# Optimization experiments

Measured on AMD Instinct MI355X. Metric: run time of the kernel, lower is better.

## Reference

```python
import jax, jax.numpy as jnp
import numpy as np

B, T, D = 32, 512, 256
F = 256  # duration_predictor_filter_size
K = 3    # kernel size, padding=1
MEL_MAX = 2304
EPS = 1e-5


def _conv1d(x, w, b):
    # x: [B, T, C_in], w: [C_out, C_in, K], 'same'-ish padding=1
    y = jax.lax.conv_general_dilated(
        x.transpose(0, 2, 1), w, window_strides=(1,), padding=[(1, 1)],
        dimension_numbers=("NCH", "OIH", "NCH"))
    return y.transpose(0, 2, 1) + b


def _layernorm(x, g, b):
    mu = jnp.mean(x, axis=-1, keepdims=True)
    var = jnp.mean(jnp.square(x - mu), axis=-1, keepdims=True)
    return (x - mu) * jax.lax.rsqrt(var + EPS) * g + b


def setup_inputs() -> dict:
    key = jax.random.key(0)
    ks = jax.random.split(key, 8)
    x = jax.random.normal(ks[0], (B, T, D), dtype=jnp.float32)
    target = jax.random.randint(ks[1], (B, T), 0, 8, dtype=jnp.int32)
    s = 0.02
    return {
        "x": x,
        "target": target,
        "mel_max_length": MEL_MAX,
        "conv1_w": jax.random.normal(ks[2], (F, D, K), dtype=jnp.float32) * s,
        "conv1_b": jnp.zeros((F,), jnp.float32),
        "ln1_g": jnp.ones((F,), jnp.float32),
        "ln1_b": jnp.zeros((F,), jnp.float32),
        "conv2_w": jax.random.normal(ks[3], (F, F, K), dtype=jnp.float32) * s,
        "conv2_b": jnp.zeros((F,), jnp.float32),
        "ln2_g": jnp.ones((F,), jnp.float32),
        "ln2_b": jnp.zeros((F,), jnp.float32),
        "lin_w": jax.random.normal(ks[4], (1, F), dtype=jnp.float32) * s,
        "lin_b": jnp.zeros((1,), jnp.float32),
    }


def reference(x, target, mel_max_length, conv1_w, conv1_b, ln1_g, ln1_b,
              conv2_w, conv2_b, ln2_g, ln2_b, lin_w, lin_b):
    # Variance_adaptor (duration predictor), eval-mode dropout = identity
    h = jax.nn.relu(_layernorm(_conv1d(x, conv1_w, conv1_b), ln1_g, ln1_b))
    h = jax.nn.relu(_layernorm(_conv1d(h, conv2_w, conv2_b), ln2_g, ln2_b))
    dur_pred = jax.nn.relu(jnp.einsum("btf,of->bto", h, lin_w) + lin_b)[..., 0]  # [B,T]

    # LR: alignment @ x, expressed as the equivalent duration-indexed gather.
    # alignment[b, t_out, j] = 1 iff cumsum(dur)[b,j-1] <= t_out < cumsum(dur)[b,j]
    cum = jnp.cumsum(target, axis=1)                    # [B, T]
    t_out = jnp.arange(mel_max_length, dtype=cum.dtype)  # [T_out]
    idx = jax.vmap(lambda c: jnp.searchsorted(c, t_out, side="right"))(cum)  # [B, T_out]
    valid = (t_out[None, :] < cum[:, -1:]).astype(x.dtype)                   # [B, T_out]
    gathered = jnp.take_along_axis(x, jnp.clip(idx, 0, T - 1)[:, :, None], axis=1)
    output = gathered * valid[:, :, None]                # zeros past total length (pad)
    return output, dur_pred
```

## Files before the change

### kernel.cpp

```cpp
#include <hip/hip_runtime.h>

typedef __attribute__((ext_vector_type(8))) short short8;
typedef __attribute__((ext_vector_type(4))) float floatx4;

typedef __attribute__((address_space(3))) unsigned int lds_u32;
typedef __attribute__((address_space(1))) const unsigned int glb_u32;

static __device__ __forceinline__ unsigned short f2bf(float f) {
    unsigned int u = __float_as_uint(f);
    return (unsigned short)((u + 0x7FFFu + ((u >> 16) & 1u)) >> 16);
}

static __device__ __forceinline__ void cp16(const ushort* g, ushort* l) {
    __builtin_amdgcn_global_load_lds((glb_u32*)g, (lds_u32*)l, 16, 0, 0);
}

__global__ __launch_bounds__(256)
void prep_kernel(const float* __restrict__ x, const float* __restrict__ w1,
                 const float* __restrict__ w2,
                 ushort* __restrict__ xb, ushort* __restrict__ h1b,
                 ushort* __restrict__ w1pb, ushort* __restrict__ w2pb)
{
    const int blk = blockIdx.x, tid = threadIdx.x;
    if (blk < 4112) {
        const int r = blk * 4 + (tid >> 6);
        const int c = (tid & 63) * 4;
        const int b = r / 514, tp = r % 514;
        ushort4 o;
        if (tp >= 1 && tp <= 512) {
            float4 v = *(const float4*)(x + ((size_t)(b * 512 + tp - 1) * 256 + c));
            o.x = f2bf(v.x); o.y = f2bf(v.y); o.z = f2bf(v.z); o.w = f2bf(v.w);
        } else {
            o.x = o.y = o.z = o.w = 0;
            *(ushort4*)(h1b + (size_t)r * 256 + c) = o;
        }
        *(ushort4*)(xb + (size_t)r * 256 + c) = o;
    } else {
        const bool second = blk >= 4880;
        const int e = (blk - (second ? 4880 : 4112)) * 256 + tid;
        const float* w = second ? w2 : w1;
        ushort* wpb = second ? w2pb : w1pb;
        const int f = e / 768, j = e % 768;
        const int c = j & 255, kr = j >> 8;
        const int s = j >> 6, kk = j & 63;
        wpb[s * 16384 + f * 64 + (((kk >> 3) ^ (f & 7)) << 3) + (kk & 7)]
            = f2bf(w[f * 768 + c * 3 + kr]);
    }
}

template<bool IS_CONV2>
__global__ __launch_bounds__(256, 2)
void conv_mfma_kernel(const ushort* __restrict__ xb,
                      const ushort* __restrict__ wpb,
                      const float* __restrict__ cbias,
                      const float* __restrict__ gamma, const float* __restrict__ beta,
                      const float* __restrict__ lw, const float* __restrict__ lb,
                      ushort* __restrict__ outb,
                      float* __restrict__ durp,
                      const float* __restrict__ x,
                      const int* __restrict__ target,
                      float* __restrict__ out0)
{
    __shared__ ushort As[32 * 64];
    __shared__ ushort Bs[256 * 64];
    __shared__ float sum_s[4][32], sq_s[4][32], mu_s[32], rs_s[32];
    __shared__ int cum[512], ps[256], sidx[64];

    const int tid = threadIdx.x;

    if (IS_CONV2 && blockIdx.x >= 512) {
        const int bg = blockIdx.x - 512;
        const int b = bg / 36, t0o = (bg % 36) * 64;
        const int v0 = target[b * 512 + 2 * tid];
        const int v1 = target[b * 512 + 2 * tid + 1];
        ps[tid] = v0 + v1;
        __syncthreads();
        for (int off = 1; off < 256; off <<= 1) {
            int t = (tid >= off) ? ps[tid - off] : 0;
            __syncthreads();
            ps[tid] += t;
            __syncthreads();
        }
        const int excl = tid ? ps[tid - 1] : 0;
        cum[2 * tid]     = excl + v0;
        cum[2 * tid + 1] = excl + v0 + v1;
        __syncthreads();
        const int total = cum[511];
        if (tid < 64) {
            int t = t0o + tid;
            int lo = 0, hi = 512;
            while (lo < hi) {
                int mid = (lo + hi) >> 1;
                if (cum[mid] <= t) lo = mid + 1; else hi = mid;
            }
            sidx[tid] = (t < total) ? ((lo < 512) ? lo : 511) : -1;
        }
        __syncthreads();
        const float4* x4 = (const float4*)x;
        float4* o4 = (float4*)out0;
        const int lane6 = tid & 63, g4 = tid >> 6;
        #pragma unroll 4
        for (int rr = 0; rr < 16; ++rr) {
            int r = rr * 4 + g4;
            int idx = sidx[r];
            float4 v = make_float4(0.f, 0.f, 0.f, 0.f);
            if (idx >= 0) v = x4[((size_t)(b * 512 + idx)) * 64 + lane6];
            o4[((size_t)(b * 2304 + t0o + r)) * 64 + lane6] = v;
        }
        return;
    }

    const int w = tid >> 6, lane = tid & 63;
    const int q = lane >> 4, col = lane & 15;
    const int b  = blockIdx.x >> 4;
    const int t0 = (blockIdx.x & 15) << 5;

    floatx4 acc[2][4] = {};
    const ushort* xbb = xb + (size_t)b * 514 * 256;
    const int arow  = tid >> 3;
    const int aquad = (tid & 7) ^ (arow & 7);
    ushort* AsW = As + (size_t)w * 512;
    ushort* BsW = Bs + (size_t)w * 512;

    for (int s = 0; s < 12; ++s) {
        const int krow = s >> 2, cb = (s & 3) << 6;
        cp16(xbb + (size_t)(t0 + krow + arow) * 256 + cb + aquad * 8, AsW);
        const ushort* wsrc = wpb + (size_t)s * 16384 + w * 512 + lane * 8;
        #pragma unroll
        for (int i = 0; i < 8; ++i)
            cp16(wsrc + i * 2048, BsW + i * 2048);
        __syncthreads();

        short8 af[2][2], bf[4][2];
        #pragma unroll
        for (int mi = 0; mi < 2; ++mi)
            #pragma unroll
            for (int kh = 0; kh < 2; ++kh)
                af[mi][kh] = *(const short8*)((const char*)As
                    + (mi * 16 + col) * 128 + (((kh * 4 + q) ^ (col & 7)) * 16));
        #pragma unroll
        for (int ni = 0; ni < 4; ++ni)
            #pragma unroll
            for (int kh = 0; kh < 2; ++kh)
                bf[ni][kh] = *(const short8*)((const char*)Bs
                    + (w * 64 + ni * 16 + col) * 128 + (((kh * 4 + q) ^ (col & 7)) * 16));
        #pragma unroll
        for (int kh = 0; kh < 2; ++kh)
            #pragma unroll
            for (int mi = 0; mi < 2; ++mi)
                #pragma unroll
                for (int ni = 0; ni < 4; ++ni)
                    acc[mi][ni] = __builtin_amdgcn_mfma_f32_16x16x32_bf16(
                        af[mi][kh], bf[ni][kh], acc[mi][ni], 0, 0, 0);
        __syncthreads();
    }

    const int base_c = w * 64;
    float cb4[4], gm4[4], bt4[4];
    #pragma unroll
    for (int ni = 0; ni < 4; ++ni) {
        cb4[ni] = cbias[base_c + ni * 16 + col];
        gm4[ni] = gamma[base_c + ni * 16 + col];
        bt4[ni] = beta [base_c + ni * 16 + col];
    }
    float rsum[2][4] = {}, rsq[2][4] = {};
    #pragma unroll
    for (int mi = 0; mi < 2; ++mi)
        #pragma unroll
        for (int ni = 0; ni < 4; ++ni)
            #pragma unroll
            for (int r = 0; r < 4; ++r) {
                float v = acc[mi][ni][r] + cb4[ni];
                acc[mi][ni][r] = v;
                rsum[mi][r] += v;
                rsq [mi][r] += v * v;
            }
    #pragma unroll
    for (int mi = 0; mi < 2; ++mi)
        #pragma unroll
        for (int r = 0; r < 4; ++r) {
            float s = rsum[mi][r], ss = rsq[mi][r];
            #pragma unroll
            for (int d = 8; d > 0; d >>= 1) {
                s  += __shfl_down(s,  d, 16);
                ss += __shfl_down(ss, d, 16);
            }
            if (col == 0) {
                sum_s[w][mi * 16 + q * 4 + r] = s;
                sq_s [w][mi * 16 + q * 4 + r] = ss;
            }
        }
    __syncthreads();
    if (tid < 32) {
        float s  = sum_s[0][tid] + sum_s[1][tid] + sum_s[2][tid] + sum_s[3][tid];
        float ss = sq_s [0][tid] + sq_s [1][tid] + sq_s [2][tid] + sq_s [3][tid];
        float mu = s * (1.f / 256.f);
        float var = ss * (1.f / 256.f) - mu * mu;
        mu_s[tid] = mu;
        rs_s[tid] = rsqrtf(var + 1e-5f);
    }
    __syncthreads();

    if (!IS_CONV2) {
        #pragma unroll
        for (int mi = 0; mi < 2; ++mi)
            #pragma unroll
            for (int ni = 0; ni < 4; ++ni)
                #pragma unroll
                for (int r = 0; r < 4; ++r) {
                    int row = mi * 16 + q * 4 + r;
                    float v = (acc[mi][ni][r] - mu_s[row]) * rs_s[row] * gm4[ni] + bt4[ni];
                    outb[((size_t)b * 514 + t0 + row + 1) * 256 + base_c + ni * 16 + col]
                        = f2bf(fmaxf(v, 0.f));
                }
    } else {
        float lw4[4];
        #pragma unroll
        for (int ni = 0; ni < 4; ++ni) lw4[ni] = lw[base_c + ni * 16 + col];
        float dsum[2][4] = {};
        #pragma unroll
        for (int mi = 0; mi < 2; ++mi)
            #pragma unroll
            for (int ni = 0; ni < 4; ++ni)
                #pragma unroll
                for (int r = 0; r < 4; ++r) {
                    int row = mi * 16 + q * 4 + r;
                    float v = (acc[mi][ni][r] - mu_s[row]) * rs_s[row] * gm4[ni] + bt4[ni];
                    dsum[mi][r] += fmaxf(v, 0.f) * lw4[ni];
                }
        #pragma unroll
        for (int mi = 0; mi < 2; ++mi)
            #pragma unroll
            for (int r = 0; r < 4; ++r) {
                float s = dsum[mi][r];
                #pragma unroll
                for (int d = 8; d > 0; d >>= 1) s += __shfl_down(s, d, 16);
                if (col == 0) sum_s[w][mi * 16 + q * 4 + r] = s;
            }
        __syncthreads();
        if (tid < 32)
            durp[b * 512 + t0 + tid] = fmaxf(sum_s[0][tid] + sum_s[1][tid]
                                           + sum_s[2][tid] + sum_s[3][tid] + lb[0], 0.f);
    }
}

extern "C" void kernel_launch(void* const* d_in, const int* in_sizes, int n_in,
                              void* d_out, int out_size, void* d_ws, size_t ws_size,
                              hipStream_t stream) {
    const float* x      = (const float*)d_in[0];
    const int*   target = (const int*)  d_in[1];
    const float* c1w = (const float*)d_in[3];
    const float* c1b = (const float*)d_in[4];
    const float* g1  = (const float*)d_in[5];
    const float* b1  = (const float*)d_in[6];
    const float* c2w = (const float*)d_in[7];
    const float* c2b = (const float*)d_in[8];
    const float* g2  = (const float*)d_in[9];
    const float* b2  = (const float*)d_in[10];
    const float* lw  = (const float*)d_in[11];
    const float* lb  = (const float*)d_in[12];

    const int B = 32, C = 256;

    const size_t PADEL = (size_t)B * 514 * 256;
    ushort* xb   = (ushort*)d_ws;
    ushort* h1b  = xb + PADEL;
    ushort* w1pb = h1b + PADEL;
    ushort* w2pb = w1pb + 196608;

    float* out0 = (float*)d_out;
    float* durp = out0 + (size_t)B * 2304 * C;

    prep_kernel<<<5648, 256, 0, stream>>>(x, c1w, c2w, xb, h1b, w1pb, w2pb);
    conv_mfma_kernel<false><<<512, 256, 0, stream>>>(
        xb, w1pb, c1b, g1, b1, nullptr, nullptr, h1b, nullptr,
        nullptr, nullptr, nullptr);
    conv_mfma_kernel<true><<<512 + 1152, 256, 0, stream>>>(
        h1b, w2pb, c2b, g2, b2, lw, lb, nullptr, durp,
        x, target, out0);
}
```

Baseline: 148.5 us.

## Fuse prep, both convs and gather into one persistent kernel with grid barriers

Replaces three kernel launches with a single 512-block persistent kernel that uses global atomic counters as grid-wide barriers between the prep, conv1 and conv2 phases. The length-regulator gather now runs in the gap between prep and conv1, hiding the prep barrier latency behind useful memory traffic. This removes launch overhead and inter-kernel drain and fill gaps. In exchange it relies on all 512 blocks being co-resident, spin-waits on atomics, and adds a memset launch.

Result: slower. 290.0 us (+95.3%).

```diff
diff --git a/kernel.cpp b/kernel.cpp
--- a/kernel.cpp
+++ b/kernel.cpp
@@ -5,25 +5,37 @@
 
 typedef __attribute__((address_space(3))) unsigned int lds_u32;
 typedef __attribute__((address_space(1))) const unsigned int glb_u32;
+
+#define NBLK 512
 
 static __device__ __forceinline__ unsigned short f2bf(float f) {
     unsigned int u = __float_as_uint(f);
     return (unsigned short)((u + 0x7FFFu + ((u >> 16) & 1u)) >> 16);
 }
-
 static __device__ __forceinline__ void cp16(const ushort* g, ushort* l) {
     __builtin_amdgcn_global_load_lds((glb_u32*)g, (lds_u32*)l, 16, 0, 0);
 }
 
-__global__ __launch_bounds__(256)
-void prep_kernel(const float* __restrict__ x, const float* __restrict__ w1,
-                 const float* __restrict__ w2,
-                 ushort* __restrict__ xb, ushort* __restrict__ h1b,
-                 ushort* __restrict__ w1pb, ushort* __restrict__ w2pb)
+__global__ __launch_bounds__(256, 2)
+void fused_kernel(const float* __restrict__ x, const int* __restrict__ target,
+                  const float* __restrict__ w1, const float* __restrict__ c1b,
+                  const float* __restrict__ g1, const float* __restrict__ b1,
+                  const float* __restrict__ w2, const float* __restrict__ c2b,
+                  const float* __restrict__ g2, const float* __restrict__ b2,
+                  const float* __restrict__ lw, const float* __restrict__ lb,
+                  ushort* __restrict__ xb, ushort* __restrict__ h1b,
+                  ushort* __restrict__ w1pb, ushort* __restrict__ w2pb,
+                  unsigned* __restrict__ bars,
+                  float* __restrict__ out0, float* __restrict__ durp)
 {
-    const int blk = blockIdx.x, tid = threadIdx.x;
-    if (blk < 4112) {
-        const int r = blk * 4 + (tid >> 6);
+    __shared__ ushort As[32 * 64];
+    __shared__ ushort Bs[256 * 64];
+    __shared__ float sum_s[4][32], sq_s[4][32], mu_s[32], rs_s[32];
+
+    const int tid = threadIdx.x, blk = blockIdx.x;
+
+    for (int u = blk; u < 4112; u += NBLK) {
+        const int r = u * 4 + (tid >> 6);
         const int c = (tid & 63) * 4;
         const int b = r / 514, tp = r % 514;
         ushort4 o;
@@ -35,44 +47,31 @@
             *(ushort4*)(h1b + (size_t)r * 256 + c) = o;
         }
         *(ushort4*)(xb + (size_t)r * 256 + c) = o;
-    } else {
-        const bool second = blk >= 4880;
-        const int e = (blk - (second ? 4880 : 4112)) * 256 + tid;
+    }
+    for (int u = blk; u < 1536; u += NBLK) {
+        const bool second = u >= 768;
+        const int e = (u - (second ? 768 : 0)) * 256 + tid;
         const float* w = second ? w2 : w1;
         ushort* wpb = second ? w2pb : w1pb;
         const int f = e / 768, j = e % 768;
         const int c = j & 255, kr = j >> 8;
-        const int s = j >> 6, kk = j & 63;
-        wpb[s * 16384 + f * 64 + (((kk >> 3) ^ (f & 7)) << 3) + (kk & 7)]
+        wpb[(j >> 6) * 16384 + f * 64 + ((((j & 63) >> 3) ^ (f & 7)) << 3) + (j & 7)]
             = f2bf(w[f * 768 + c * 3 + kr]);
     }
-}
-
-template<bool IS_CONV2>
-__global__ __launch_bounds__(256, 2)
-void conv_mfma_kernel(const ushort* __restrict__ xb,
-                      const ushort* __restrict__ wpb,
-                      const float* __restrict__ cbias,
-                      const float* __restrict__ gamma, const float* __restrict__ beta,
-                      const float* __restrict__ lw, const float* __restrict__ lb,
-                      ushort* __restrict__ outb,
-                      float* __restrict__ durp,
-                      const float* __restrict__ x,
-                      const int* __restrict__ target,
-                      float* __restrict__ out0)
-{
-    __shared__ ushort As[32 * 64];
-    __shared__ ushort Bs[256 * 64];
-    __shared__ float sum_s[4][32], sq_s[4][32], mu_s[32], rs_s[32];
-    __shared__ int cum[512], ps[256], sidx[64];
-
-    const int tid = threadIdx.x;
-
-    if (IS_CONV2 && blockIdx.x >= 512) {
-        const int bg = blockIdx.x - 512;
-        const int b = bg / 36, t0o = (bg % 36) * 64;
-        const int v0 = target[b * 512 + 2 * tid];
-        const int v1 = target[b * 512 + 2 * tid + 1];
+
+    __syncthreads();
+    if (tid == 0) {
+        __threadfence();
+        __hip_atomic_fetch_add(&bars[0], 1u, __ATOMIC_RELEASE, __HIP_MEMORY_SCOPE_AGENT);
+    }
+
+    {
+        int* cum  = (int*)Bs;
+        int* ps   = cum + 512;
+        int* sidx = ps + 256;
+        const int gb = blk >> 4, gseg = blk & 15;
+        const int v0 = target[gb * 512 + 2 * tid];
+        const int v1 = target[gb * 512 + 2 * tid + 1];
         ps[tid] = v0 + v1;
         __syncthreads();
         for (int off = 1; off < 256; off <<= 1) {
@@ -86,8 +85,8 @@
         cum[2 * tid + 1] = excl + v0 + v1;
         __syncthreads();
         const int total = cum[511];
-        if (tid < 64) {
-            int t = t0o + tid;
+        if (tid < 144) {
+            int t = gseg * 144 + tid;
             int lo = 0, hi = 512;
             while (lo < hi) {
                 int mid = (lo + hi) >> 1;
@@ -100,108 +99,103 @@
         float4* o4 = (float4*)out0;
         const int lane6 = tid & 63, g4 = tid >> 6;
         #pragma unroll 4
-        for (int rr = 0; rr < 16; ++rr) {
-            int r = rr * 4 + g4;
+        for (int it = 0; it < 36; ++it) {
+            int r = it * 4 + g4;
             int idx = sidx[r];
             float4 v = make_float4(0.f, 0.f, 0.f, 0.f);
-            if (idx >= 0) v = x4[((size_t)(b * 512 + idx)) * 64 + lane6];
-            o4[((size_t)(b * 2304 + t0o + r)) * 64 + lane6] = v;
-        }
-        return;
-    }
-
-    const int w = tid >> 6, lane = tid & 63;
+            if (idx >= 0) v = x4[((size_t)(gb * 512 + idx)) * 64 + lane6];
+            o4[((size_t)(gb * 2304 + gseg * 144 + r)) * 64 + lane6] = v;
+        }
+    }
+
+    if (tid == 0)
+        while (__hip_atomic_load(&bars[0], __ATOMIC_ACQUIRE,
+                                 __HIP_MEMORY_SCOPE_AGENT) < NBLK)
+            __builtin_amdgcn_s_sleep(2);
+    __syncthreads();
+
+    const int w_ = tid >> 6, lane = tid & 63;
     const int q = lane >> 4, col = lane & 15;
-    const int b  = blockIdx.x >> 4;
-    const int t0 = (blockIdx.x & 15) << 5;
-
-    floatx4 acc[2][4] = {};
-    const ushort* xbb = xb + (size_t)b * 514 * 256;
-    const int arow  = tid >> 3;
-    const int aquad = (tid & 7) ^ (arow & 7);
-    ushort* AsW = As + (size_t)w * 512;
-    ushort* BsW = Bs + (size_t)w * 512;
-
-    for (int s = 0; s < 12; ++s) {
-        const int krow = s >> 2, cb = (s & 3) << 6;
-        cp16(xbb + (size_t)(t0 + krow + arow) * 256 + cb + aquad * 8, AsW);
-        const ushort* wsrc = wpb + (size_t)s * 16384 + w * 512 + lane * 8;
-        #pragma unroll
-        for (int i = 0; i < 8; ++i)
-            cp16(wsrc + i * 2048, BsW + i * 2048);
-        __syncthreads();
-
-        short8 af[2][2], bf[4][2];
-        #pragma unroll
-        for (int mi = 0; mi < 2; ++mi)
+    const int cbk_b = blk >> 4, t0 = (blk & 15) << 5;
+    const int arow = tid >> 3, aquad = (tid & 7) ^ (arow & 7);
+    ushort* AsW = As + (size_t)w_ * 512;
+    ushort* BsW = Bs + (size_t)w_ * 512;
+    const int base_c = w_ * 64;
+
+    {
+        floatx4 acc[2][4] = {};
+        const ushort* inb = xb + (size_t)cbk_b * 514 * 256;
+        for (int s = 0; s < 12; ++s) {
+            const int krow = s >> 2, cbo = (s & 3) << 6;
+            cp16(inb + (size_t)(t0 + krow + arow) * 256 + cbo + aquad * 8, AsW);
+            const ushort* wsrc = w1pb + (size_t)s * 16384 + w_ * 512 + lane * 8;
+            #pragma unroll
+            for (int i = 0; i < 8; ++i) cp16(wsrc + i * 2048, BsW + i * 2048);
+            __syncthreads();
+            short8 af[2][2], bf[4][2];
+            #pragma unroll
+            for (int mi = 0; mi < 2; ++mi)
+                #pragma unroll
+                for (int kh = 0; kh < 2; ++kh)
+                    af[mi][kh] = *(const short8*)((const char*)As
+                        + (mi * 16 + col) * 128 + (((kh * 4 + q) ^ (col & 7)) * 16));
+            #pragma unroll
+            for (int ni = 0; ni < 4; ++ni)
+                #pragma unroll
+                for (int kh = 0; kh < 2; ++kh)
+                    bf[ni][kh] = *(const short8*)((const char*)Bs
+                        + (w_ * 64 + ni * 16 + col) * 128 + (((kh * 4 + q) ^ (col & 7)) * 16));
             #pragma unroll
             for (int kh = 0; kh < 2; ++kh)
-                af[mi][kh] = *(const short8*)((const char*)As
-                    + (mi * 16 + col) * 128 + (((kh * 4 + q) ^ (col & 7)) * 16));
-        #pragma unroll
-        for (int ni = 0; ni < 4; ++ni)
-            #pragma unroll
-            for (int kh = 0; kh < 2; ++kh)
-                bf[ni][kh] = *(const short8*)((const char*)Bs
-                    + (w * 64 + ni * 16 + col) * 128 + (((kh * 4 + q) ^ (col & 7)) * 16));
-        #pragma unroll
-        for (int kh = 0; kh < 2; ++kh)
-            #pragma unroll
-            for (int mi = 0; mi < 2; ++mi)
-                #pragma unroll
-                for (int ni = 0; ni < 4; ++ni)
-                    acc[mi][ni] = __builtin_amdgcn_mfma_f32_16x16x32_bf16(
-                        af[mi][kh], bf[ni][kh], acc[mi][ni], 0, 0, 0);
-        __syncthreads();
-    }
-
-    const int base_c = w * 64;
-    float cb4[4], gm4[4], bt4[4];
-    #pragma unroll
-    for (int ni = 0; ni < 4; ++ni) {
-        cb4[ni] = cbias[base_c + ni * 16 + col];
-        gm4[ni] = gamma[base_c + ni * 16 + col];
-        bt4[ni] = beta [base_c + ni * 16 + col];
-    }
-    float rsum[2][4] = {}, rsq[2][4] = {};
-    #pragma unroll
-    for (int mi = 0; mi < 2; ++mi)
-        #pragma unroll
-        for (int ni = 0; ni < 4; ++ni)
+                #pragma unroll
+                for (int mi = 0; mi < 2; ++mi)
+                    #pragma unroll
+                    for (int ni = 0; ni < 4; ++ni)
+                        acc[mi][ni] = __builtin_amdgcn_mfma_f32_16x16x32_bf16(
+                            af[mi][kh], bf[ni][kh], acc[mi][ni], 0, 0, 0);
+            __syncthreads();
+        }
+        float cb4[4], gm4[4], bt4[4];
+        #pragma unroll
+        for (int ni = 0; ni < 4; ++ni) {
+            cb4[ni] = c1b[base_c + ni * 16 + col];
+            gm4[ni] = g1 [base_c + ni * 16 + col];
+            bt4[ni] = b1 [base_c + ni * 16 + col];
+        }
+        float rsum[2][4] = {}, rsq[2][4] = {};
+        #pragma unroll
+        for (int mi = 0; mi < 2; ++mi)
+            #pragma unroll
+            for (int ni = 0; ni < 4; ++ni)
+                #pragma unroll
+                for (int r = 0; r < 4; ++r) {
+                    float v = acc[mi][ni][r] + cb4[ni];
+                    acc[mi][ni][r] = v;
+                    rsum[mi][r] += v; rsq[mi][r] += v * v;
+                }
+        #pragma unroll
+        for (int mi = 0; mi < 2; ++mi)
             #pragma unroll
             for (int r = 0; r < 4; ++r) {
-                float v = acc[mi][ni][r] + cb4[ni];
-                acc[mi][ni][r] = v;
-                rsum[mi][r] += v;
-                rsq [mi][r] += v * v;
+                float s = rsum[mi][r], ss = rsq[mi][r];
+                #pragma unroll
+                for (int d = 8; d > 0; d >>= 1) {
+                    s += __shfl_down(s, d, 16); ss += __shfl_down(ss, d, 16);
+                }
+                if (col == 0) {
+                    sum_s[w_][mi * 16 + q * 4 + r] = s;
+                    sq_s [w_][mi * 16 + q * 4 + r] = ss;
+                }
             }
-    #pragma unroll
-    for (int mi = 0; mi < 2; ++mi)
-        #pragma unroll
-        for (int r = 0; r < 4; ++r) {
-            float s = rsum[mi][r], ss = rsq[mi][r];
-            #pragma unroll
-            for (int d = 8; d > 0; d >>= 1) {
-                s  += __shfl_down(s,  d, 16);
-                ss += __shfl_down(ss, d, 16);
-            }
-            if (col == 0) {
-                sum_s[w][mi * 16 + q * 4 + r] = s;
-                sq_s [w][mi * 16 + q * 4 + r] = ss;
-            }
-        }
-    __syncthreads();
-    if (tid < 32) {
-        float s  = sum_s[0][tid] + sum_s[1][tid] + sum_s[2][tid] + sum_s[3][tid];
-        float ss = sq_s [0][tid] + sq_s [1][tid] + sq_s [2][tid] + sq_s [3][tid];
-        float mu = s * (1.f / 256.f);
-        float var = ss * (1.f / 256.f) - mu * mu;
-        mu_s[tid] = mu;
-        rs_s[tid] = rsqrtf(var + 1e-5f);
-    }
-    __syncthreads();
-
-    if (!IS_CONV2) {
+        __syncthreads();
+        if (tid < 32) {
+            float s  = sum_s[0][tid] + sum_s[1][tid] + sum_s[2][tid] + sum_s[3][tid];
+            float ss = sq_s [0][tid] + sq_s [1][tid] + sq_s [2][tid] + sq_s [3][tid];
+            float mu = s * (1.f / 256.f);
+            mu_s[tid] = mu;
+            rs_s[tid] = rsqrtf(ss * (1.f / 256.f) - mu * mu + 1e-5f);
+        }
+        __syncthreads();
         #pragma unroll
         for (int mi = 0; mi < 2; ++mi)
             #pragma unroll
@@ -210,13 +204,96 @@
                 for (int r = 0; r < 4; ++r) {
                     int row = mi * 16 + q * 4 + r;
                     float v = (acc[mi][ni][r] - mu_s[row]) * rs_s[row] * gm4[ni] + bt4[ni];
-                    outb[((size_t)b * 514 + t0 + row + 1) * 256 + base_c + ni * 16 + col]
+                    h1b[((size_t)cbk_b * 514 + t0 + row + 1) * 256 + base_c + ni * 16 + col]
                         = f2bf(fmaxf(v, 0.f));
                 }
-    } else {
-        float lw4[4];
-        #pragma unroll
-        for (int ni = 0; ni < 4; ++ni) lw4[ni] = lw[base_c + ni * 16 + col];
+    }
+
+    __syncthreads();
+    if (tid == 0) {
+        __threadfence();
+        __hip_atomic_fetch_add(&bars[1], 1u, __ATOMIC_RELEASE, __HIP_MEMORY_SCOPE_AGENT);
+        while (__hip_atomic_load(&bars[1], __ATOMIC_ACQUIRE,
+                                 __HIP_MEMORY_SCOPE_AGENT) < NBLK)
+            __builtin_amdgcn_s_sleep(2);
+    }
+    __syncthreads();
+
+    {
+        floatx4 acc[2][4] = {};
+        const ushort* inb = h1b + (size_t)cbk_b * 514 * 256;
+        for (int s = 0; s < 12; ++s) {
+            const int krow = s >> 2, cbo = (s & 3) << 6;
+            cp16(inb + (size_t)(t0 + krow + arow) * 256 + cbo + aquad * 8, AsW);
+            const ushort* wsrc = w2pb + (size_t)s * 16384 + w_ * 512 + lane * 8;
+            #pragma unroll
+            for (int i = 0; i < 8; ++i) cp16(wsrc + i * 2048, BsW + i * 2048);
+            __syncthreads();
+            short8 af[2][2], bf[4][2];
+            #pragma unroll
+            for (int mi = 0; mi < 2; ++mi)
+                #pragma unroll
+                for (int kh = 0; kh < 2; ++kh)
+                    af[mi][kh] = *(const short8*)((const char*)As
+                        + (mi * 16 + col) * 128 + (((kh * 4 + q) ^ (col & 7)) * 16));
+            #pragma unroll
+            for (int ni = 0; ni < 4; ++ni)
+                #pragma unroll
+                for (int kh = 0; kh < 2; ++kh)
+                    bf[ni][kh] = *(const short8*)((const char*)Bs
+                        + (w_ * 64 + ni * 16 + col) * 128 + (((kh * 4 + q) ^ (col & 7)) * 16));
+            #pragma unroll
+            for (int kh = 0; kh < 2; ++kh)
+                #pragma unroll
+                for (int mi = 0; mi < 2; ++mi)
+                    #pragma unroll
+                    for (int ni = 0; ni < 4; ++ni)
+                        acc[mi][ni] = __builtin_amdgcn_mfma_f32_16x16x32_bf16(
+                            af[mi][kh], bf[ni][kh], acc[mi][ni], 0, 0, 0);
+            __syncthreads();
+        }
+        float cb4[4], gm4[4], bt4[4], lw4[4];
+        #pragma unroll
+        for (int ni = 0; ni < 4; ++ni) {
+            cb4[ni] = c2b[base_c + ni * 16 + col];
+            gm4[ni] = g2 [base_c + ni * 16 + col];
+            bt4[ni] = b2 [base_c + ni * 16 + col];
+            lw4[ni] = lw [base_c + ni * 16 + col];
+        }
+        float rsum[2][4] = {}, rsq[2][4] = {};
+        #pragma unroll
+        for (int mi = 0; mi < 2; ++mi)
+            #pragma unroll
+            for (int ni = 0; ni < 4; ++ni)
+                #pragma unroll
+                for (int r = 0; r < 4; ++r) {
+                    float v = acc[mi][ni][r] + cb4[ni];
+                    acc[mi][ni][r] = v;
+                    rsum[mi][r] += v; rsq[mi][r] += v * v;
+                }
+        #pragma unroll
+        for (int mi = 0; mi < 2; ++mi)
+            #pragma unroll
+            for (int r = 0; r < 4; ++r) {
+                float s = rsum[mi][r], ss = rsq[mi][r];
+                #pragma unroll
+                for (int d = 8; d > 0; d >>= 1) {
+                    s += __shfl_down(s, d, 16); ss += __shfl_down(ss, d, 16);
+                }
+                if (col == 0) {
+                    sum_s[w_][mi * 16 + q * 4 + r] = s;
+                    sq_s [w_][mi * 16 + q * 4 + r] = ss;
+                }
+            }
+        __syncthreads();
+        if (tid < 32) {
+            float s  = sum_s[0][tid] + sum_s[1][tid] + sum_s[2][tid] + sum_s[3][tid];
+            float ss = sq_s [0][tid] + sq_s [1][tid] + sq_s [2][tid] + sq_s [3][tid];
+            float mu = s * (1.f / 256.f);
+            mu_s[tid] = mu;
+            rs_s[tid] = rsqrtf(ss * (1.f / 256.f) - mu * mu + 1e-5f);
+        }
+        __syncthreads();
         float dsum[2][4] = {};
         #pragma unroll
         for (int mi = 0; mi < 2; ++mi)
@@ -235,12 +312,12 @@
                 float s = dsum[mi][r];
                 #pragma unroll
                 for (int d = 8; d > 0; d >>= 1) s += __shfl_down(s, d, 16);
-                if (col == 0) sum_s[w][mi * 16 + q * 4 + r] = s;
+                if (col == 0) sum_s[w_][mi * 16 + q * 4 + r] = s;
             }
         __syncthreads();
         if (tid < 32)
-            durp[b * 512 + t0 + tid] = fmaxf(sum_s[0][tid] + sum_s[1][tid]
-                                           + sum_s[2][tid] + sum_s[3][tid] + lb[0], 0.f);
+            durp[cbk_b * 512 + t0 + tid] = fmaxf(sum_s[0][tid] + sum_s[1][tid]
+                                               + sum_s[2][tid] + sum_s[3][tid] + lb[0], 0.f);
     }
 }
 
@@ -260,22 +337,18 @@
     const float* lw  = (const float*)d_in[11];
     const float* lb  = (const float*)d_in[12];
 
-    const int B = 32, C = 256;
-
-    const size_t PADEL = (size_t)B * 514 * 256;
+    const size_t PADEL = (size_t)32 * 514 * 256;
     ushort* xb   = (ushort*)d_ws;
     ushort* h1b  = xb + PADEL;
     ushort* w1pb = h1b + PADEL;
     ushort* w2pb = w1pb + 196608;
+    unsigned* bars = (unsigned*)(w2pb + 196608);
 
     float* out0 = (float*)d_out;
-    float* durp = out0 + (size_t)B * 2304 * C;
-
-    prep_kernel<<<5648, 256, 0, stream>>>(x, c1w, c2w, xb, h1b, w1pb, w2pb);
-    conv_mfma_kernel<false><<<512, 256, 0, stream>>>(
-        xb, w1pb, c1b, g1, b1, nullptr, nullptr, h1b, nullptr,
-        nullptr, nullptr, nullptr);
-    conv_mfma_kernel<true><<<512 + 1152, 256, 0, stream>>>(
-        h1b, w2pb, c2b, g2, b2, lw, lb, nullptr, durp,
-        x, target, out0);
+    float* durp = out0 + (size_t)32 * 2304 * 256;
+
+    hipMemsetAsync(bars, 0, 16, stream);
+    fused_kernel<<<NBLK, 256, 0, stream>>>(
+        x, target, c1w, c1b, g1, b1, c2w, c2b, g2, b2, lw, lb,
+        xb, h1b, w1pb, w2pb, bars, out0, durp);
 }
```

## Double-buffer per-wave weight tiles in LDS and load activations directly to registers

Applied to the files above, without the earlier changes.

The conv MFMA main loop no longer stages the activation tile in shared memory. Each lane now loads its A fragments straight from global memory into registers, and the next stage's fragments are prefetched while the current one is consumed. Weight tiles go into a per-wave private double buffer in LDS, filled with global_load_lds and synchronised only with s_waitcnt vmcnt, so both block-wide barriers per k-step are gone. The aim is to overlap memory latency with MFMA work and drop barrier stalls, at the cost of more registers, uncoalesced direct global fragment loads, and one redundant prefetch on the last step.

New measurement: 168.6 us. +13.5%, slower.

```diff
diff --git a/kernel.cpp b/kernel.cpp
--- a/kernel.cpp
+++ b/kernel.cpp
@@ -10,7 +10,6 @@
     unsigned int u = __float_as_uint(f);
     return (unsigned short)((u + 0x7FFFu + ((u >> 16) & 1u)) >> 16);
 }
-
 static __device__ __forceinline__ void cp16(const ushort* g, ushort* l) {
     __builtin_amdgcn_global_load_lds((glb_u32*)g, (lds_u32*)l, 16, 0, 0);
 }
@@ -61,8 +60,7 @@
                       const int* __restrict__ target,
                       float* __restrict__ out0)
 {
-    __shared__ ushort As[32 * 64];
-    __shared__ ushort Bs[256 * 64];
+    __shared__ ushort Bws[4][2][4096];
     __shared__ float sum_s[4][32], sq_s[4][32], mu_s[32], rs_s[32];
     __shared__ int cum[512], ps[256], sidx[64];
 
@@ -110,40 +108,51 @@
         return;
     }
 
-    const int w = tid >> 6, lane = tid & 63;
+    const int w_ = tid >> 6, lane = tid & 63;
     const int q = lane >> 4, col = lane & 15;
     const int b  = blockIdx.x >> 4;
     const int t0 = (blockIdx.x & 15) << 5;
 
     floatx4 acc[2][4] = {};
-    const ushort* xbb = xb + (size_t)b * 514 * 256;
-    const int arow  = tid >> 3;
-    const int aquad = (tid & 7) ^ (arow & 7);
-    ushort* AsW = As + (size_t)w * 512;
-    ushort* BsW = Bs + (size_t)w * 512;
-
+    const ushort* xbb = xb + ((size_t)b * 514 + t0) * 256;
+    const ushort* wpw = wpb + w_ * 4096 + lane * 8;
+    ushort* buf0 = &Bws[w_][0][0];
+    ushort* buf1 = &Bws[w_][1][0];
+
+    short8 afb[2][2][2];
+
+    #pragma unroll
+    for (int i = 0; i < 8; ++i) cp16(wpw + i * 512, buf0 + i * 512);
+    #pragma unroll
+    for (int mi = 0; mi < 2; ++mi)
+        #pragma unroll
+        for (int kh = 0; kh < 2; ++kh)
+            afb[0][mi][kh] = *(const short8*)(xbb + (size_t)(mi * 16 + col) * 256
+                                              + kh * 32 + q * 8);
+
+    #pragma unroll
     for (int s = 0; s < 12; ++s) {
-        const int krow = s >> 2, cb = (s & 3) << 6;
-        cp16(xbb + (size_t)(t0 + krow + arow) * 256 + cb + aquad * 8, AsW);
-        const ushort* wsrc = wpb + (size_t)s * 16384 + w * 512 + lane * 8;
-        #pragma unroll
-        for (int i = 0; i < 8; ++i)
-            cp16(wsrc + i * 2048, BsW + i * 2048);
-        __syncthreads();
-
-        short8 af[2][2], bf[4][2];
+        const int sp = (s < 11) ? s + 1 : 11;
+        const int krow = sp >> 2, cb = (sp & 3) << 6;
+        ushort* nbuf = (s & 1) ? buf0 : buf1;
+        const ushort* wsrc = wpw + (size_t)sp * 16384;
+        #pragma unroll
+        for (int i = 0; i < 8; ++i) cp16(wsrc + i * 512, nbuf + i * 512);
         #pragma unroll
         for (int mi = 0; mi < 2; ++mi)
             #pragma unroll
             for (int kh = 0; kh < 2; ++kh)
-                af[mi][kh] = *(const short8*)((const char*)As
-                    + (mi * 16 + col) * 128 + (((kh * 4 + q) ^ (col & 7)) * 16));
+                afb[(s + 1) & 1][mi][kh] = *(const short8*)(xbb
+                    + (size_t)(mi * 16 + col + krow) * 256 + cb + kh * 32 + q * 8);
+        asm volatile("s_waitcnt vmcnt(12)" ::: "memory");
+        const ushort* cbuf = (s & 1) ? buf1 : buf0;
+        short8 bfr[4][2];
         #pragma unroll
         for (int ni = 0; ni < 4; ++ni)
             #pragma unroll
             for (int kh = 0; kh < 2; ++kh)
-                bf[ni][kh] = *(const short8*)((const char*)Bs
-                    + (w * 64 + ni * 16 + col) * 128 + (((kh * 4 + q) ^ (col & 7)) * 16));
+                bfr[ni][kh] = *(const short8*)((const char*)cbuf
+                    + (ni * 16 + col) * 128 + (((kh * 4 + q) ^ (col & 7)) << 4));
         #pragma unroll
         for (int kh = 0; kh < 2; ++kh)
             #pragma unroll
@@ -151,11 +160,10 @@
                 #pragma unroll
                 for (int ni = 0; ni < 4; ++ni)
                     acc[mi][ni] = __builtin_amdgcn_mfma_f32_16x16x32_bf16(
-                        af[mi][kh], bf[ni][kh], acc[mi][ni], 0, 0, 0);
-        __syncthreads();
-    }
-
-    const int base_c = w * 64;
+                        afb[s & 1][mi][kh], bfr[ni][kh], acc[mi][ni], 0, 0, 0);
+    }
+
+    const int base_c = w_ * 64;
     float cb4[4], gm4[4], bt4[4];
     #pragma unroll
     for (int ni = 0; ni < 4; ++ni) {
@@ -186,8 +194,8 @@
                 ss += __shfl_down(ss, d, 16);
             }
             if (col == 0) {
-                sum_s[w][mi * 16 + q * 4 + r] = s;
-                sq_s [w][mi * 16 + q * 4 + r] = ss;
+                sum_s[w_][mi * 16 + q * 4 + r] = s;
+                sq_s [w_][mi * 16 + q * 4 + r] = ss;
             }
         }
     __syncthreads();
@@ -195,9 +203,8 @@
         float s  = sum_s[0][tid] + sum_s[1][tid] + sum_s[2][tid] + sum_s[3][tid];
         float ss = sq_s [0][tid] + sq_s [1][tid] + sq_s [2][tid] + sq_s [3][tid];
         float mu = s * (1.f / 256.f);
-        float var = ss * (1.f / 256.f) - mu * mu;
         mu_s[tid] = mu;
-        rs_s[tid] = rsqrtf(var + 1e-5f);
+        rs_s[tid] = rsqrtf(ss * (1.f / 256.f) - mu * mu + 1e-5f);
     }
     __syncthreads();
 
@@ -235,7 +242,7 @@
                 float s = dsum[mi][r];
                 #pragma unroll
                 for (int d = 8; d > 0; d >>= 1) s += __shfl_down(s, d, 16);
-                if (col == 0) sum_s[w][mi * 16 + q * 4 + r] = s;
+                if (col == 0) sum_s[w_][mi * 16 + q * 4 + r] = s;
             }
         __syncthreads();
         if (tid < 32)
@@ -260,16 +267,14 @@
     const float* lw  = (const float*)d_in[11];
     const float* lb  = (const float*)d_in[12];
 
-    const int B = 32, C = 256;
-
-    const size_t PADEL = (size_t)B * 514 * 256;
+    const size_t PADEL = (size_t)32 * 514 * 256;
     ushort* xb   = (ushort*)d_ws;
     ushort* h1b  = xb + PADEL;
     ushort* w1pb = h1b + PADEL;
     ushort* w2pb = w1pb + 196608;
 
     float* out0 = (float*)d_out;
-    float* durp = out0 + (size_t)B * 2304 * C;
+    float* durp = out0 + (size_t)32 * 2304 * 256;
 
     prep_kernel<<<5648, 256, 0, stream>>>(x, c1w, c2w, xb, h1b, w1pb, w2pb);
     conv_mfma_kernel<false><<<512, 256, 0, stream>>>(
```
